# Kernel optimization log

Measured on AMD Instinct MI355X. Metric: run time of the kernel, lower is better.

Reference implementation:

```python
import jax, jax.numpy as jnp
import numpy as np

N_NODES = 100_000
N_EDGES = 1_600_000
HIDDEN = 128
OUT_DIM = 400


def setup_inputs() -> dict:
    key = jax.random.key(0)
    ks = jax.random.split(key, 6)
    x = jax.random.normal(ks[0], (N_NODES, 1), dtype=jnp.float32)
    edge_index = jax.random.randint(ks[1], (2, N_EDGES), 0, N_NODES, dtype=jnp.int32)
    # Glorot-style init for the two GCN weight matrices
    W1 = jax.random.normal(ks[2], (1, HIDDEN), dtype=jnp.float32) * (1.0 / np.sqrt(1 + HIDDEN))
    b1 = jnp.zeros((HIDDEN,), dtype=jnp.float32)
    W2 = jax.random.normal(ks[3], (HIDDEN, OUT_DIM), dtype=jnp.float32) * (1.0 / np.sqrt(HIDDEN + OUT_DIM))
    b2 = jnp.zeros((OUT_DIM,), dtype=jnp.float32)
    return {"x": x, "edge_index": edge_index, "W1": W1, "b1": b1, "W2": W2, "b2": b2}


def _gcn_layer(x, W, b, row, col, norm, num_nodes):
    # PyG GCNConv: out[col] += norm * (x @ W)[row]; then + bias
    h = x @ W                                   # [N, F_out]
    msg = h[row] * norm[:, None]                # [E+N, F_out] gather + scale
    out = jax.ops.segment_sum(msg, col, num_segments=num_nodes)  # scatter-add
    return out + b


def reference(x, edge_index, W1, b1, W2, b2):
    n = x.shape[0]
    loops = jnp.arange(n, dtype=edge_index.dtype)
    row = jnp.concatenate([edge_index[0], loops])  # sources (+ self loops)
    col = jnp.concatenate([edge_index[1], loops])  # destinations (+ self loops)
    # symmetric normalization: deg over destinations, norm = d^-1/2[row] * d^-1/2[col]
    deg = jnp.zeros((n,), dtype=x.dtype).at[col].add(1.0)  # >=1 due to self loops
    dinv = jax.lax.rsqrt(deg)
    norm = dinv[row] * dinv[col]
    h = jax.nn.relu(_gcn_layer(x, W1, b1, row, col, norm, n))
    h = _gcn_layer(h, W2, b2, row, col, norm, n)
    return h.mean(axis=0)  # [OUT_DIM]
```

## Files before the change

### kernel.cpp

```cpp
#include <hip/hip_runtime.h>
#include <math.h>


constexpr int BKT_BITS = 12;
constexpr int BKT_SIZE = 1 << BKT_BITS;
constexpr int NBMAX    = 32;
constexpr int CSTR     = 64;
constexpr int CAP      = 67584;
constexpr int SLICES   = 12;
constexpr int SLICES_D = 24;
constexpr int EPT      = 4;
constexpr int NSLOT    = 32;

__global__ void init_misc(int* __restrict__ curC, int* __restrict__ curR,
                          float* __restrict__ tslot, unsigned* __restrict__ cnt) {
    int t = threadIdx.x;
    if (t < NBMAX) { curC[t * CSTR] = 0; curR[t * CSTR] = 0; }
    for (int j = t; j < NSLOT * 128; j += 256) tslot[j] = 0.0f;
    if (t == 0) *cnt = 0u;
}

__global__ void scatter_edges(const int* __restrict__ row, const int* __restrict__ col,
                              int* __restrict__ SC, int* __restrict__ SR,
                              int* __restrict__ curC, int* __restrict__ curR, int E) {
    __shared__ int hC[NBMAX], hR[NBMAX], bC[NBMAX], bR[NBMAX];
    const int TILE = blockDim.x * EPT;
    const int myBase = blockIdx.x * TILE + threadIdx.x * EPT;
    int r[EPT], c[EPT];
    if (myBase + EPT <= E) {
        int4 r0 = *reinterpret_cast<const int4*>(row + myBase);
        int4 c0 = *reinterpret_cast<const int4*>(col + myBase);
        r[0]=r0.x; r[1]=r0.y; r[2]=r0.z; r[3]=r0.w;
        c[0]=c0.x; c[1]=c0.y; c[2]=c0.z; c[3]=c0.w;
    } else {
#pragma unroll
        for (int j = 0; j < EPT; ++j) {
            int e = myBase + j;
            r[j] = (e < E) ? row[e] : -1;
            c[j] = (e < E) ? col[e] : -1;
        }
    }
    if (threadIdx.x < NBMAX) { hC[threadIdx.x] = 0; hR[threadIdx.x] = 0; }
    __syncthreads();
    int offC[EPT], offR[EPT];
#pragma unroll
    for (int j = 0; j < EPT; ++j) {
        if (r[j] >= 0) {
            offC[j] = atomicAdd(&hC[c[j] >> BKT_BITS], 1);
            offR[j] = atomicAdd(&hR[r[j] >> BKT_BITS], 1);
        }
    }
    __syncthreads();
    if (threadIdx.x < NBMAX) {
        bC[threadIdx.x] = atomicAdd(&curC[threadIdx.x * CSTR], hC[threadIdx.x]);
        bR[threadIdx.x] = atomicAdd(&curR[threadIdx.x * CSTR], hR[threadIdx.x]);
    }
    __syncthreads();
#pragma unroll
    for (int j = 0; j < EPT; ++j) {
        if (r[j] >= 0) {
            int kb = c[j] >> BKT_BITS;
            int idx = kb * CAP + bC[kb] + offC[j];
            if (idx < (kb + 1) * CAP)
                SC[idx] = ((c[j] & (BKT_SIZE - 1)) << 17) | r[j];
            int kb2 = r[j] >> BKT_BITS;
            int idx2 = kb2 * CAP + bR[kb2] + offR[j];
            if (idx2 < (kb2 + 1) * CAP)
                SR[idx2] = ((r[j] & (BKT_SIZE - 1)) << 17) | c[j];
        }
    }
}

__global__ void hist_deg(const int* __restrict__ SC, const int* __restrict__ cur,
                         float* __restrict__ P, int stride) {
    __shared__ float bins[BKT_SIZE];
    const int b = blockIdx.x / SLICES_D, s = blockIdx.x % SLICES_D;
    const int base = b * CAP;
    int len = cur[b * CSTR];
    len = len < CAP ? len : CAP;
    const int lo = base + (int)((long long)len * s / SLICES_D);
    const int hi = base + (int)((long long)len * (s + 1) / SLICES_D);
    for (int i = threadIdx.x; i < BKT_SIZE; i += blockDim.x) bins[i] = 0.0f;
    __syncthreads();
    for (int e = lo + threadIdx.x; e < hi; e += blockDim.x)
        atomicAdd(&bins[SC[e] >> 17], 1.0f);
    __syncthreads();
    float* dst = P + (size_t)s * stride + b * BKT_SIZE;
    for (int i = threadIdx.x; i < BKT_SIZE; i += blockDim.x) dst[i] = bins[i];
}

__global__ void finalize_deg(const float* __restrict__ Pd, const float* __restrict__ x,
                             float* __restrict__ dinv, float* __restrict__ u,
                             int N, int stride) {
    int i = blockIdx.x * blockDim.x + threadIdx.x;
    if (i >= N) return;
    float d = 1.0f;
    for (int s = 0; s < SLICES_D; ++s) d += Pd[(size_t)s * stride + i];
    float di = rsqrtf(d);
    dinv[i] = di;
    u[i] = di * x[i];
}

__global__ void hist_gather_both(const int* __restrict__ SC, const int* __restrict__ SR,
                                 const int* __restrict__ curC, const int* __restrict__ curR,
                                 const float* __restrict__ u, const float* __restrict__ dinv,
                                 float* __restrict__ Ps, float* __restrict__ Pw,
                                 int stride, int half) {
    __shared__ float bins[BKT_SIZE];
    const bool isW = blockIdx.x >= half;
    const int id = isW ? blockIdx.x - half : blockIdx.x;
    const int* S = isW ? SR : SC;
    const int* cur = isW ? curR : curC;
    const float* val = isW ? dinv : u;
    float* P = isW ? Pw : Ps;
    const int b = id / SLICES, s = id % SLICES;
    const int base = b * CAP;
    int len = cur[b * CSTR];
    len = len < CAP ? len : CAP;
    const int lo = base + (int)((long long)len * s / SLICES);
    const int hi = base + (int)((long long)len * (s + 1) / SLICES);
    for (int i = threadIdx.x; i < BKT_SIZE; i += blockDim.x) bins[i] = 0.0f;
    __syncthreads();
    for (int e = lo + threadIdx.x; e < hi; e += blockDim.x) {
        int v = S[e];
        atomicAdd(&bins[v >> 17], val[v & 0x1FFFF]);
    }
    __syncthreads();
    float* dst = P + (size_t)s * stride + b * BKT_SIZE;
    for (int i = threadIdx.x; i < BKT_SIZE; i += blockDim.x) dst[i] = bins[i];
}

__global__ void fused_node(const float* __restrict__ Ps, const float* __restrict__ Pw,
                           const float* __restrict__ dinv, const float* __restrict__ x,
                           const float* __restrict__ W1, const float* __restrict__ b1,
                           float* __restrict__ tslot, int N, int stride,
                           const float* __restrict__ W2, const float* __restrict__ b2,
                           float* __restrict__ out, int OUT, float invN,
                           unsigned* __restrict__ cnt) {
    __shared__ float scs[256];
    __shared__ float ws[256];
    __shared__ float red[256];
    __shared__ unsigned lastFlag;
    const int tid = threadIdx.x;
    const int i = blockIdx.x * 256 + tid;
    float scv = 0.0f, wv = 0.0f;
    if (i < N) {
        float sr = 0.0f, wr = 0.0f;
        for (int s = 0; s < SLICES; ++s) {
            sr += Ps[(size_t)s * stride + i];
            wr += Pw[(size_t)s * stride + i];
        }
        float di = dinv[i];
        scv = di * sr + di * di * x[i];
        wv  = di * (wr + di);
    }
    scs[tid] = scv;
    ws[tid]  = wv;
    __syncthreads();
    const int k = tid & 127;
    const int base = (tid >> 7) * 128;
    const float w1k = W1[k];
    const float b1k = b1[k];
    float acc = 0.0f;
#pragma unroll 4
    for (int j = 0; j < 128; ++j) {
        float h = scs[base + j] * w1k + b1k;
        h = h > 0.0f ? h : 0.0f;
        acc += ws[base + j] * h;
    }
    red[tid] = acc;
    __syncthreads();
    if (tid < 128)
        atomicAdd(&tslot[(blockIdx.x & (NSLOT - 1)) * 128 + k],
                  red[tid] + red[tid + 128]);
    __syncthreads();
    if (tid == 0)
        lastFlag = (atomicAdd(cnt, 1u) == (unsigned)(gridDim.x - 1)) ? 1u : 0u;
    __syncthreads();
    if (lastFlag) {
        __shared__ float tv[128];
        if (tid < 128) {
            float s = 0.0f;
#pragma unroll
            for (int g = 0; g < NSLOT; ++g)
                s += atomicAdd(&tslot[g * 128 + tid], 0.0f);
            tv[tid] = s * invN;
        }
        __syncthreads();
        for (int d = tid; d < OUT; d += 256) {
            float a = b2[d];
#pragma unroll 4
            for (int kk = 0; kk < 128; ++kk) a += tv[kk] * W2[kk * OUT + d];
            out[d] = a;
        }
    }
}

extern "C" void kernel_launch(void* const* d_in, const int* in_sizes, int n_in,
                              void* d_out, int out_size, void* d_ws, size_t ws_size,
                              hipStream_t stream) {
    const float* x          = (const float*)d_in[0];
    const int*   edge_index = (const int*)  d_in[1];
    const float* W1         = (const float*)d_in[2];
    const float* b1         = (const float*)d_in[3];
    const float* W2         = (const float*)d_in[4];
    const float* b2         = (const float*)d_in[5];
    float* out = (float*)d_out;

    const int N   = in_sizes[0];
    const int E   = in_sizes[1] / 2;
    const int OUT = in_sizes[5];

    const int* row = edge_index;
    const int* col = edge_index + E;

    const int NB = (N + BKT_SIZE - 1) >> BKT_BITS;
    const int stride = NB * BKT_SIZE;

    char* p = (char*)d_ws;
    float* dinv  = (float*)p; p += (size_t)N * 4;
    float* u     = (float*)p; p += (size_t)N * 4;
    float* tslot = (float*)p; p += (size_t)NSLOT * 128 * 4;
    int*   ints  = (int*)p;   p += (size_t)(2 * NBMAX * CSTR + CSTR) * 4;
    int*   SC    = (int*)p;   p += (size_t)NB * CAP * 4;
    int*   SR    = (int*)p;   p += (size_t)NB * CAP * 4;
    float* P     = (float*)p;
    float* Ps    = P;
    float* Pw    = P + (size_t)SLICES * stride;

    int* curC = ints;
    int* curR = ints + NBMAX * CSTR;
    unsigned* cnt = (unsigned*)(ints + 2 * NBMAX * CSTR);

    const int TILE   = 256 * EPT;
    const int nTiles = (E + TILE - 1) / TILE;

    init_misc<<<1, 256, 0, stream>>>(curC, curR, tslot, cnt);
    scatter_edges<<<nTiles, 256, 0, stream>>>(row, col, SC, SR, curC, curR, E);
    hist_deg<<<NB * SLICES_D, 256, 0, stream>>>(SC, curC, P, stride);
    finalize_deg<<<(N + 255) / 256, 256, 0, stream>>>(P, x, dinv, u, N, stride);
    const int half = NB * SLICES;
    hist_gather_both<<<2 * half, 256, 0, stream>>>(SC, SR, curC, curR, u, dinv,
                                                   Ps, Pw, stride, half);
    fused_node<<<(N + 255) / 256, 256, 0, stream>>>(Ps, Pw, dinv, x, W1, b1,
                                                    tslot, N, stride,
                                                    W2, b2, out, OUT,
                                                    1.0f / (float)N, cnt);
}
```

Measured before the change: 189.9 us.

## Fuse all GCN stages into one cooperative persistent kernel with grid syncs

Replaces the five separate kernel launches (scatter, degree histogram, finalize, gather histograms, node reduction) with a single cooperative kernel. It runs a persistent grid of at most 1024 blocks and separates the stages with grid-wide syncs. The aim is to remove launch gaps and tail effects between stages, and to drop the atomic last-block counter. In exchange, each stage now loops over work with fewer blocks than before, and every stage boundary costs a grid barrier. The grid is capped at 1024 blocks, which may cut the parallelism available to the scatter and histogram phases.

```diff
diff --git a/kernel.cpp b/kernel.cpp
--- a/kernel.cpp
+++ b/kernel.cpp
@@ -1,5 +1,8 @@
 #include <hip/hip_runtime.h>
+#include <hip/hip_cooperative_groups.h>
 #include <math.h>
+
+namespace cg = cooperative_groups;
 
 
 constexpr int BKT_BITS = 12;
@@ -13,177 +16,181 @@
 constexpr int NSLOT    = 32;
 
 __global__ void init_misc(int* __restrict__ curC, int* __restrict__ curR,
-                          float* __restrict__ tslot, unsigned* __restrict__ cnt) {
+                          float* __restrict__ tslot) {
     int t = threadIdx.x;
     if (t < NBMAX) { curC[t * CSTR] = 0; curR[t * CSTR] = 0; }
     for (int j = t; j < NSLOT * 128; j += 256) tslot[j] = 0.0f;
-    if (t == 0) *cnt = 0u;
 }
 
-__global__ void scatter_edges(const int* __restrict__ row, const int* __restrict__ col,
-                              int* __restrict__ SC, int* __restrict__ SR,
-                              int* __restrict__ curC, int* __restrict__ curR, int E) {
-    __shared__ int hC[NBMAX], hR[NBMAX], bC[NBMAX], bR[NBMAX];
-    const int TILE = blockDim.x * EPT;
-    const int myBase = blockIdx.x * TILE + threadIdx.x * EPT;
-    int r[EPT], c[EPT];
-    if (myBase + EPT <= E) {
-        int4 r0 = *reinterpret_cast<const int4*>(row + myBase);
-        int4 c0 = *reinterpret_cast<const int4*>(col + myBase);
-        r[0]=r0.x; r[1]=r0.y; r[2]=r0.z; r[3]=r0.w;
-        c[0]=c0.x; c[1]=c0.y; c[2]=c0.z; c[3]=c0.w;
-    } else {
-#pragma unroll
-        for (int j = 0; j < EPT; ++j) {
-            int e = myBase + j;
-            r[j] = (e < E) ? row[e] : -1;
-            c[j] = (e < E) ? col[e] : -1;
-        }
-    }
-    if (threadIdx.x < NBMAX) { hC[threadIdx.x] = 0; hR[threadIdx.x] = 0; }
-    __syncthreads();
-    int offC[EPT], offR[EPT];
-#pragma unroll
-    for (int j = 0; j < EPT; ++j) {
-        if (r[j] >= 0) {
-            offC[j] = atomicAdd(&hC[c[j] >> BKT_BITS], 1);
-            offR[j] = atomicAdd(&hR[r[j] >> BKT_BITS], 1);
-        }
-    }
-    __syncthreads();
-    if (threadIdx.x < NBMAX) {
-        bC[threadIdx.x] = atomicAdd(&curC[threadIdx.x * CSTR], hC[threadIdx.x]);
-        bR[threadIdx.x] = atomicAdd(&curR[threadIdx.x * CSTR], hR[threadIdx.x]);
-    }
-    __syncthreads();
-#pragma unroll
-    for (int j = 0; j < EPT; ++j) {
-        if (r[j] >= 0) {
-            int kb = c[j] >> BKT_BITS;
-            int idx = kb * CAP + bC[kb] + offC[j];
-            if (idx < (kb + 1) * CAP)
-                SC[idx] = ((c[j] & (BKT_SIZE - 1)) << 17) | r[j];
-            int kb2 = r[j] >> BKT_BITS;
-            int idx2 = kb2 * CAP + bR[kb2] + offR[j];
-            if (idx2 < (kb2 + 1) * CAP)
-                SR[idx2] = ((r[j] & (BKT_SIZE - 1)) << 17) | c[j];
-        }
-    }
-}
-
-__global__ void hist_deg(const int* __restrict__ SC, const int* __restrict__ cur,
-                         float* __restrict__ P, int stride) {
+__global__ __launch_bounds__(256, 8)
+void mega(const int* __restrict__ row, const int* __restrict__ col,
+          int* __restrict__ SC, int* __restrict__ SR,
+          int* __restrict__ curC, int* __restrict__ curR,
+          const float* __restrict__ x, const float* __restrict__ W1,
+          const float* __restrict__ b1, const float* __restrict__ W2,
+          const float* __restrict__ b2, float* __restrict__ dinv,
+          float* __restrict__ u, float* __restrict__ Ps, float* __restrict__ Pw,
+          float* __restrict__ tslot, float* __restrict__ out,
+          int E, int N, int OUT, int stride, float invN)
+{
+    cg::grid_group grid = cg::this_grid();
     __shared__ float bins[BKT_SIZE];
-    const int b = blockIdx.x / SLICES_D, s = blockIdx.x % SLICES_D;
-    const int base = b * CAP;
-    int len = cur[b * CSTR];
-    len = len < CAP ? len : CAP;
-    const int lo = base + (int)((long long)len * s / SLICES_D);
-    const int hi = base + (int)((long long)len * (s + 1) / SLICES_D);
-    for (int i = threadIdx.x; i < BKT_SIZE; i += blockDim.x) bins[i] = 0.0f;
-    __syncthreads();
-    for (int e = lo + threadIdx.x; e < hi; e += blockDim.x)
-        atomicAdd(&bins[SC[e] >> 17], 1.0f);
-    __syncthreads();
-    float* dst = P + (size_t)s * stride + b * BKT_SIZE;
-    for (int i = threadIdx.x; i < BKT_SIZE; i += blockDim.x) dst[i] = bins[i];
-}
-
-__global__ void finalize_deg(const float* __restrict__ Pd, const float* __restrict__ x,
-                             float* __restrict__ dinv, float* __restrict__ u,
-                             int N, int stride) {
-    int i = blockIdx.x * blockDim.x + threadIdx.x;
-    if (i >= N) return;
-    float d = 1.0f;
-    for (int s = 0; s < SLICES_D; ++s) d += Pd[(size_t)s * stride + i];
-    float di = rsqrtf(d);
-    dinv[i] = di;
-    u[i] = di * x[i];
-}
-
-__global__ void hist_gather_both(const int* __restrict__ SC, const int* __restrict__ SR,
-                                 const int* __restrict__ curC, const int* __restrict__ curR,
-                                 const float* __restrict__ u, const float* __restrict__ dinv,
-                                 float* __restrict__ Ps, float* __restrict__ Pw,
-                                 int stride, int half) {
-    __shared__ float bins[BKT_SIZE];
-    const bool isW = blockIdx.x >= half;
-    const int id = isW ? blockIdx.x - half : blockIdx.x;
-    const int* S = isW ? SR : SC;
-    const int* cur = isW ? curR : curC;
-    const float* val = isW ? dinv : u;
-    float* P = isW ? Pw : Ps;
-    const int b = id / SLICES, s = id % SLICES;
-    const int base = b * CAP;
-    int len = cur[b * CSTR];
-    len = len < CAP ? len : CAP;
-    const int lo = base + (int)((long long)len * s / SLICES);
-    const int hi = base + (int)((long long)len * (s + 1) / SLICES);
-    for (int i = threadIdx.x; i < BKT_SIZE; i += blockDim.x) bins[i] = 0.0f;
-    __syncthreads();
-    for (int e = lo + threadIdx.x; e < hi; e += blockDim.x) {
-        int v = S[e];
-        atomicAdd(&bins[v >> 17], val[v & 0x1FFFF]);
-    }
-    __syncthreads();
-    float* dst = P + (size_t)s * stride + b * BKT_SIZE;
-    for (int i = threadIdx.x; i < BKT_SIZE; i += blockDim.x) dst[i] = bins[i];
-}
-
-__global__ void fused_node(const float* __restrict__ Ps, const float* __restrict__ Pw,
-                           const float* __restrict__ dinv, const float* __restrict__ x,
-                           const float* __restrict__ W1, const float* __restrict__ b1,
-                           float* __restrict__ tslot, int N, int stride,
-                           const float* __restrict__ W2, const float* __restrict__ b2,
-                           float* __restrict__ out, int OUT, float invN,
-                           unsigned* __restrict__ cnt) {
-    __shared__ float scs[256];
-    __shared__ float ws[256];
-    __shared__ float red[256];
-    __shared__ unsigned lastFlag;
     const int tid = threadIdx.x;
-    const int i = blockIdx.x * 256 + tid;
-    float scv = 0.0f, wv = 0.0f;
-    if (i < N) {
-        float sr = 0.0f, wr = 0.0f;
-        for (int s = 0; s < SLICES; ++s) {
-            sr += Ps[(size_t)s * stride + i];
-            wr += Pw[(size_t)s * stride + i];
-        }
-        float di = dinv[i];
-        scv = di * sr + di * di * x[i];
-        wv  = di * (wr + di);
-    }
-    scs[tid] = scv;
-    ws[tid]  = wv;
-    __syncthreads();
-    const int k = tid & 127;
-    const int base = (tid >> 7) * 128;
-    const float w1k = W1[k];
-    const float b1k = b1[k];
-    float acc = 0.0f;
+    const int NB = (N + BKT_SIZE - 1) >> BKT_BITS;
+
+    {
+        int* hC = (int*)bins; int* hR = hC + NBMAX;
+        int* bC = hR + NBMAX; int* bR = bC + NBMAX;
+        const int TILE = 256 * EPT;
+        const int nT = (E + TILE - 1) / TILE;
+        for (int t = blockIdx.x; t < nT; t += gridDim.x) {
+            const int myBase = t * TILE + tid * EPT;
+            int r[EPT], c[EPT];
+            if (myBase + EPT <= E) {
+                int4 r0 = *reinterpret_cast<const int4*>(row + myBase);
+                int4 c0 = *reinterpret_cast<const int4*>(col + myBase);
+                r[0]=r0.x; r[1]=r0.y; r[2]=r0.z; r[3]=r0.w;
+                c[0]=c0.x; c[1]=c0.y; c[2]=c0.z; c[3]=c0.w;
+            } else {
+#pragma unroll
+                for (int j = 0; j < EPT; ++j) {
+                    int e = myBase + j;
+                    r[j] = (e < E) ? row[e] : -1;
+                    c[j] = (e < E) ? col[e] : -1;
+                }
+            }
+            if (tid < NBMAX) { hC[tid] = 0; hR[tid] = 0; }
+            __syncthreads();
+            int offC[EPT], offR[EPT];
+#pragma unroll
+            for (int j = 0; j < EPT; ++j) {
+                if (r[j] >= 0) {
+                    offC[j] = atomicAdd(&hC[c[j] >> BKT_BITS], 1);
+                    offR[j] = atomicAdd(&hR[r[j] >> BKT_BITS], 1);
+                }
+            }
+            __syncthreads();
+            if (tid < NBMAX) {
+                bC[tid] = atomicAdd(&curC[tid * CSTR], hC[tid]);
+                bR[tid] = atomicAdd(&curR[tid * CSTR], hR[tid]);
+            }
+            __syncthreads();
+#pragma unroll
+            for (int j = 0; j < EPT; ++j) {
+                if (r[j] >= 0) {
+                    int kb = c[j] >> BKT_BITS;
+                    int idx = kb * CAP + bC[kb] + offC[j];
+                    if (idx < (kb + 1) * CAP)
+                        SC[idx] = ((c[j] & (BKT_SIZE - 1)) << 17) | r[j];
+                    int kb2 = r[j] >> BKT_BITS;
+                    int idx2 = kb2 * CAP + bR[kb2] + offR[j];
+                    if (idx2 < (kb2 + 1) * CAP)
+                        SR[idx2] = ((r[j] & (BKT_SIZE - 1)) << 17) | c[j];
+                }
+            }
+            __syncthreads();
+        }
+    }
+    grid.sync();
+
+    for (int v = blockIdx.x; v < NB * SLICES_D; v += gridDim.x) {
+        const int b = v / SLICES_D, s = v % SLICES_D;
+        const int base = b * CAP;
+        int len = curC[b * CSTR]; len = len < CAP ? len : CAP;
+        const int lo = base + (int)((long long)len * s / SLICES_D);
+        const int hi = base + (int)((long long)len * (s + 1) / SLICES_D);
+        for (int i = tid; i < BKT_SIZE; i += 256) bins[i] = 0.0f;
+        __syncthreads();
+        for (int e = lo + tid; e < hi; e += 256)
+            atomicAdd(&bins[SC[e] >> 17], 1.0f);
+        __syncthreads();
+        float* dst = Ps + (size_t)s * stride + b * BKT_SIZE;
+        for (int i = tid; i < BKT_SIZE; i += 256) dst[i] = bins[i];
+        __syncthreads();
+    }
+    grid.sync();
+
+    for (int i = blockIdx.x * 256 + tid; i < N; i += gridDim.x * 256) {
+        float d = 1.0f;
+        for (int s = 0; s < SLICES_D; ++s) d += Ps[(size_t)s * stride + i];
+        float di = rsqrtf(d);
+        dinv[i] = di;
+        u[i] = di * x[i];
+    }
+    grid.sync();
+
+    const int half = NB * SLICES;
+    for (int v = blockIdx.x; v < 2 * half; v += gridDim.x) {
+        const bool isW = v >= half;
+        const int id = isW ? v - half : v;
+        const int* S = isW ? SR : SC;
+        const int* cur = isW ? curR : curC;
+        const float* val = isW ? dinv : u;
+        float* P = isW ? Pw : Ps;
+        const int b = id / SLICES, s = id % SLICES;
+        const int base = b * CAP;
+        int len = cur[b * CSTR]; len = len < CAP ? len : CAP;
+        const int lo = base + (int)((long long)len * s / SLICES);
+        const int hi = base + (int)((long long)len * (s + 1) / SLICES);
+        for (int i = tid; i < BKT_SIZE; i += 256) bins[i] = 0.0f;
+        __syncthreads();
+        for (int e = lo + tid; e < hi; e += 256) {
+            int w = S[e];
+            atomicAdd(&bins[w >> 17], val[w & 0x1FFFF]);
+        }
+        __syncthreads();
+        float* dst = P + (size_t)s * stride + b * BKT_SIZE;
+        for (int i = tid; i < BKT_SIZE; i += 256) dst[i] = bins[i];
+        __syncthreads();
+    }
+    grid.sync();
+
+    {
+        float* scs = bins; float* ws = bins + 256; float* red = bins + 512;
+        const int nT5 = (N + 255) / 256;
+        for (int v = blockIdx.x; v < nT5; v += gridDim.x) {
+            const int i = v * 256 + tid;
+            float scv = 0.0f, wv = 0.0f;
+            if (i < N) {
+                float sr = 0.0f, wr = 0.0f;
+                for (int s = 0; s < SLICES; ++s) {
+                    sr += Ps[(size_t)s * stride + i];
+                    wr += Pw[(size_t)s * stride + i];
+                }
+                float di = dinv[i];
+                scv = di * sr + di * di * x[i];
+                wv  = di * (wr + di);
+            }
+            scs[tid] = scv;
+            ws[tid]  = wv;
+            __syncthreads();
+            const int k = tid & 127;
+            const int kb = (tid >> 7) * 128;
+            const float w1k = W1[k];
+            const float b1k = b1[k];
+            float acc = 0.0f;
 #pragma unroll 4
-    for (int j = 0; j < 128; ++j) {
-        float h = scs[base + j] * w1k + b1k;
-        h = h > 0.0f ? h : 0.0f;
-        acc += ws[base + j] * h;
-    }
-    red[tid] = acc;
-    __syncthreads();
-    if (tid < 128)
-        atomicAdd(&tslot[(blockIdx.x & (NSLOT - 1)) * 128 + k],
-                  red[tid] + red[tid + 128]);
-    __syncthreads();
-    if (tid == 0)
-        lastFlag = (atomicAdd(cnt, 1u) == (unsigned)(gridDim.x - 1)) ? 1u : 0u;
-    __syncthreads();
-    if (lastFlag) {
-        __shared__ float tv[128];
+            for (int j = 0; j < 128; ++j) {
+                float h = scs[kb + j] * w1k + b1k;
+                h = h > 0.0f ? h : 0.0f;
+                acc += ws[kb + j] * h;
+            }
+            red[tid] = acc;
+            __syncthreads();
+            if (tid < 128)
+                atomicAdd(&tslot[(v & (NSLOT - 1)) * 128 + k],
+                          red[tid] + red[tid + 128]);
+            __syncthreads();
+        }
+    }
+    grid.sync();
+
+    if (blockIdx.x == 0) {
+        float* tv = bins;
         if (tid < 128) {
             float s = 0.0f;
 #pragma unroll
-            for (int g = 0; g < NSLOT; ++g)
-                s += atomicAdd(&tslot[g * 128 + tid], 0.0f);
+            for (int g = 0; g < NSLOT; ++g) s += tslot[g * 128 + tid];
             tv[tid] = s * invN;
         }
         __syncthreads();
@@ -199,23 +206,25 @@
 extern "C" void kernel_launch(void* const* d_in, const int* in_sizes, int n_in,
                               void* d_out, int out_size, void* d_ws, size_t ws_size,
                               hipStream_t stream) {
-    const float* x          = (const float*)d_in[0];
-    const int*   edge_index = (const int*)  d_in[1];
-    const float* W1         = (const float*)d_in[2];
-    const float* b1         = (const float*)d_in[3];
-    const float* W2         = (const float*)d_in[4];
-    const float* b2         = (const float*)d_in[5];
+    const int*   row_p;
+    const int*   col_p;
+    const float* x  = (const float*)d_in[0];
+    const int*   edge_index = (const int*)d_in[1];
+    const float* W1 = (const float*)d_in[2];
+    const float* b1 = (const float*)d_in[3];
+    const float* W2 = (const float*)d_in[4];
+    const float* b2 = (const float*)d_in[5];
     float* out = (float*)d_out;
 
-    const int N   = in_sizes[0];
-    const int E   = in_sizes[1] / 2;
-    const int OUT = in_sizes[5];
-
-    const int* row = edge_index;
-    const int* col = edge_index + E;
+    int N   = in_sizes[0];
+    int E   = in_sizes[1] / 2;
+    int OUT = in_sizes[5];
+
+    row_p = edge_index;
+    col_p = edge_index + E;
 
     const int NB = (N + BKT_SIZE - 1) >> BKT_BITS;
-    const int stride = NB * BKT_SIZE;
+    int stride = NB * BKT_SIZE;
 
     char* p = (char*)d_ws;
     float* dinv  = (float*)p; p += (size_t)N * 4;
@@ -230,20 +239,25 @@
 
     int* curC = ints;
     int* curR = ints + NBMAX * CSTR;
-    unsigned* cnt = (unsigned*)(ints + 2 * NBMAX * CSTR);
-
-    const int TILE   = 256 * EPT;
-    const int nTiles = (E + TILE - 1) / TILE;
-
-    init_misc<<<1, 256, 0, stream>>>(curC, curR, tslot, cnt);
-    scatter_edges<<<nTiles, 256, 0, stream>>>(row, col, SC, SR, curC, curR, E);
-    hist_deg<<<NB * SLICES_D, 256, 0, stream>>>(SC, curC, P, stride);
-    finalize_deg<<<(N + 255) / 256, 256, 0, stream>>>(P, x, dinv, u, N, stride);
-    const int half = NB * SLICES;
-    hist_gather_both<<<2 * half, 256, 0, stream>>>(SC, SR, curC, curR, u, dinv,
-                                                   Ps, Pw, stride, half);
-    fused_node<<<(N + 255) / 256, 256, 0, stream>>>(Ps, Pw, dinv, x, W1, b1,
-                                                    tslot, N, stride,
-                                                    W2, b2, out, OUT,
-                                                    1.0f / (float)N, cnt);
+
+    static int coop_grid = -1;
+    if (coop_grid < 0) {
+        int bpc = 0;
+        if (hipOccupancyMaxActiveBlocksPerMultiprocessor(
+                &bpc, reinterpret_cast<const void*>(&mega), 256, 0) != hipSuccess
+            || bpc < 1)
+            bpc = 2;
+        coop_grid = bpc * 256;
+        if (coop_grid > 1024) coop_grid = 1024;
+    }
+
+    float invN = 1.0f / (float)N;
+    void* kargs[] = {&row_p, &col_p, &SC, &SR, &curC, &curR,
+                     &x, &W1, &b1, &W2, &b2,
+                     &dinv, &u, &Ps, &Pw, &tslot, &out,
+                     &E, &N, &OUT, &stride, &invN};
+
+    init_misc<<<1, 256, 0, stream>>>(curC, curR, tslot);
+    hipLaunchCooperativeKernel(reinterpret_cast<const void*>(&mega),
+                               dim3(coop_grid), dim3(256), kargs, 0, stream);
 }
```

Result: slower. 720.0 us (+279.0%).
